# Optimization experiments

Hardware: AMD Instinct MI355X
Metric: run time of the kernel (lower is better)

Reference implementation:

```python
import jax, jax.numpy as jnp
import numpy as np

NUM_NODES = 100000
NUM_EDGES = 640000
IN_DIM = 128
OUT_DIM = 128
NUM_REL = 16


def setup_inputs() -> dict:
    key = jax.random.key(0)
    k1, k2, k3, k4, k5 = jax.random.split(key, 5)
    x = jax.random.normal(k1, (NUM_NODES, IN_DIM), dtype=jnp.float32)
    edge_index = jax.random.randint(k2, (2, NUM_EDGES), 0, NUM_NODES, dtype=jnp.int64)
    edge_types = jax.random.randint(k3, (NUM_EDGES,), 0, NUM_REL, dtype=jnp.int64)
    # xavier-uniform-ish params
    rw_bound = float(np.sqrt(6.0 / (IN_DIM * OUT_DIM + NUM_REL)))
    relation_weights = jax.random.uniform(k4, (NUM_REL, IN_DIM, OUT_DIM), dtype=jnp.float32, minval=-rw_bound, maxval=rw_bound)
    sw_bound = float(np.sqrt(6.0 / (IN_DIM + OUT_DIM)))
    self_weight = jax.random.uniform(k5, (IN_DIM, OUT_DIM), dtype=jnp.float32, minval=-sw_bound, maxval=sw_bound)
    bias = jnp.zeros((OUT_DIM,), dtype=jnp.float32)
    return {
        'x': x,
        'edge_index': edge_index,
        'edge_types': edge_types,
        'relation_weights': relation_weights,
        'self_weight': self_weight,
        'bias': bias,
    }


def reference(x, edge_index, edge_types, relation_weights, self_weight, bias):
    num_nodes = x.shape[0]
    # self loop transform: (N, out)
    self_msg = x @ self_weight
    # transform all nodes by every relation weight once: (R, N, out)
    transformed = jnp.einsum('ni,rio->rno', x, relation_weights)
    src = edge_index[0]
    dst = edge_index[1]
    # per-edge message: pick (relation, source) transformed feature -> (E, out)
    msgs = transformed[edge_types, src]
    # scatter-add into destination nodes
    neighbor_msg = jax.ops.segment_sum(msgs, dst, num_segments=num_nodes)
    # dropout=0.0 (eval) -> identity
    return jax.nn.relu(self_msg + neighbor_msg + bias)
```

## Files before the change

kernel.cpp:

```cpp
#include <hip/hip_runtime.h>

#define N_NODES 100000
#define N_EDGES 640000
#define IN_DIM  128
#define OUT_DIM 128
#define N_REL   16
#define EPB     64
#define MEPB    128
#define PAD     2048
#define NB_SCAN ((N_NODES + 255) / 256)
#define CVT_XB  (N_NODES * IN_DIM / 4 / 256)
#define CVT_WB  (17 * 16384 / 256)
#define HIST_B  ((N_EDGES + 255) / 256)

typedef unsigned short u16;
typedef unsigned int   u32;
typedef __attribute__((ext_vector_type(8))) short bf16x8;
typedef __attribute__((ext_vector_type(4))) float f32x4;

__device__ inline u16 f2bf(float f) {
    u32 u = __builtin_bit_cast(u32, f);
    return (u16)((u + 0x7fffu + ((u >> 16) & 1u)) >> 16);
}
__device__ inline float bf2f(u16 s) {
    u32 u = ((u32)s) << 16;
    return __builtin_bit_cast(float, u);
}

__global__ __launch_bounds__(256) void k_pre(const float* __restrict__ x,
                                             const float* __restrict__ rw,
                                             const float* __restrict__ sw,
                                             const int* __restrict__ etype,
                                             const int* __restrict__ dst,
                                             u16* __restrict__ xb,
                                             u16* __restrict__ wt,
                                             int* __restrict__ counts_rel,
                                             int* __restrict__ dst_count) {
    int b = blockIdx.x, t = threadIdx.x;
    if (b < CVT_XB) {
        int i = b * 256 + t;
        float4 v = ((const float4*)x)[i];
        ushort4 p; p.x = f2bf(v.x); p.y = f2bf(v.y); p.z = f2bf(v.z); p.w = f2bf(v.w);
        ((ushort4*)xb)[i] = p;
    } else if (b < CVT_XB + CVT_WB) {
        int i = (b - CVT_XB) * 256 + t;
        int r = i >> 14, rem = i & 16383, n = rem & 127;
        float v = (r < 16) ? rw[i] : sw[rem];
        int k = rem >> 7;
        wt[(size_t)r * 16384 + n * 128 + k] = f2bf(v);
    } else {
        __shared__ int bins[N_REL];
        if (t < N_REL) bins[t] = 0;
        __syncthreads();
        int e = (b - CVT_XB - CVT_WB) * 256 + t;
        if (e < N_EDGES) {
            atomicAdd(&bins[etype[e]], 1);
            atomicAdd(&dst_count[dst[e]], 1);
        }
        __syncthreads();
        if (t < N_REL && bins[t]) atomicAdd(&counts_rel[t], bins[t]);
    }
}

__global__ __launch_bounds__(256) void k_scan1(const int* __restrict__ dst_count,
                                               int* __restrict__ row_ptr,
                                               int* __restrict__ part) {
    __shared__ int buf[2][256];
    int t = threadIdx.x;
    int i = blockIdx.x * 256 + t;
    int v = (i < N_NODES) ? dst_count[i] : 0;
    buf[0][t] = v;
    __syncthreads();
    int cur = 0;
    #pragma unroll
    for (int off = 1; off < 256; off <<= 1) {
        int nxt = cur ^ 1;
        int s = buf[cur][t];
        if (t >= off) s += buf[cur][t - off];
        buf[nxt][t] = s;
        __syncthreads();
        cur = nxt;
    }
    int inc = buf[cur][t];
    if (i < N_NODES) row_ptr[i] = inc - v;
    if (t == 255) part[blockIdx.x] = inc;
}

__global__ __launch_bounds__(512) void k_mid2(int* __restrict__ part,
                                              const int* __restrict__ counts,
                                              int* __restrict__ cursor,
                                              int* __restrict__ seg,
                                              int* __restrict__ sorted) {
    int t = threadIdx.x;
    if (blockIdx.x == 0) {
        __shared__ int buf[2][512];
        int v = (t < NB_SCAN) ? part[t] : 0;
        buf[0][t] = v;
        __syncthreads();
        int cur = 0;
        #pragma unroll
        for (int off = 1; off < 512; off <<= 1) {
            int nxt = cur ^ 1;
            int s = buf[cur][t];
            if (t >= off) s += buf[cur][t - off];
            buf[nxt][t] = s;
            __syncthreads();
            cur = nxt;
        }
        int inc = buf[cur][t];
        if (t < NB_SCAN) part[t] = inc - v;
    } else {
        __shared__ int s_seg[N_REL + 1];
        if (t == 0) {
            int s = 0;
            for (int r = 0; r < N_REL; ++r) {
                cursor[r] = s; seg[r] = s; s_seg[r] = s;
                s += (counts[r] + 127) & ~127;
            }
            seg[N_REL] = s; s_seg[N_REL] = s;
        }
        __syncthreads();
        for (int r = 0; r < N_REL; ++r) {
            int b = s_seg[r] + counts[r], e2 = s_seg[r + 1];
            if (b + t < e2) sorted[b + t] = N_EDGES + r;
        }
        for (int i = s_seg[N_REL] + t; i < N_EDGES + PAD; i += 512)
            sorted[i] = N_EDGES + (N_REL - 1);
    }
}

__global__ __launch_bounds__(256) void k_scan3(int* __restrict__ row_ptr,
                                               const int* __restrict__ part,
                                               int* __restrict__ cursor_dst) {
    int t = threadIdx.x;
    int i = blockIdx.x * 256 + t;
    if (i < N_NODES) {
        int r = row_ptr[i] + part[blockIdx.x];
        row_ptr[i] = r;
        cursor_dst[i] = r;
    }
    if (i == 0) row_ptr[N_NODES] = N_EDGES;
}

__global__ __launch_bounds__(256) void k_scatter_pos(const int* __restrict__ etype,
                                                     const int* __restrict__ dst,
                                                     int* __restrict__ cursor_rel,
                                                     int* __restrict__ cursor_dst,
                                                     int* __restrict__ sorted,
                                                     int* __restrict__ pos) {
    __shared__ int bins[N_REL];
    __shared__ int base[N_REL];
    int t = threadIdx.x;
    if (t < N_REL) bins[t] = 0;
    __syncthreads();
    int e = blockIdx.x * 256 + t;
    int rel = 0;
    bool valid = (e < N_EDGES);
    if (valid) { rel = etype[e]; atomicAdd(&bins[rel], 1); }
    __syncthreads();
    if (t < N_REL) {
        base[t] = bins[t] ? atomicAdd(&cursor_rel[t], bins[t]) : 0;
        bins[t] = 0;
    }
    __syncthreads();
    if (valid) {
        int slot = base[rel] + atomicAdd(&bins[rel], 1);
        sorted[slot] = e;
        pos[slot] = atomicAdd(&cursor_dst[dst[e]], 1);
    }
}

__global__ __launch_bounds__(256, 4) void k_self_mfma(const u16* __restrict__ xb,
                                                      const u16* __restrict__ wt,
                                                      const float* __restrict__ bias,
                                                      float* __restrict__ out) {
    int t = threadIdx.x;
    int w = t >> 6, lane = t & 63;
    int n = lane & 15, q = lane >> 4;
    int n0 = blockIdx.x * 256 + w * 64;
    const u16* wr = wt + (size_t)16 * 16384;

    bf16x8 bx[4][4];
    int node[4];
    #pragma unroll
    for (int g = 0; g < 4; ++g) {
        node[g] = n0 + g * 16 + n;
        int rn = node[g] < N_NODES ? node[g] : N_NODES - 1;
        const u16* xrow = xb + (size_t)rn * 128 + q * 8;
        #pragma unroll
        for (int kk = 0; kk < 4; ++kk)
            bx[g][kk] = *(const bf16x8*)(xrow + kk * 32);
    }
    #pragma unroll
    for (int c = 0; c < 8; ++c) {
        bf16x8 aw[4];
        const u16* wrow = wr + (c * 16 + n) * 128 + q * 8;
        #pragma unroll
        for (int kk = 0; kk < 4; ++kk)
            aw[kk] = *(const bf16x8*)(wrow + kk * 32);
        float4 b4 = *(const float4*)&bias[c * 16 + q * 4];
        #pragma unroll
        for (int g = 0; g < 4; ++g) {
            f32x4 acc = {0.f, 0.f, 0.f, 0.f};
            #pragma unroll
            for (int kk = 0; kk < 4; ++kk)
                acc = __builtin_amdgcn_mfma_f32_16x16x32_bf16(aw[kk], bx[g][kk], acc, 0, 0, 0);
            if (node[g] < N_NODES) {
                float4 o;
                o.x = acc[0] + b4.x; o.y = acc[1] + b4.y;
                o.z = acc[2] + b4.z; o.w = acc[3] + b4.w;
                *(float4*)&out[(size_t)node[g] * 128 + c * 16 + q * 4] = o;
            }
        }
    }
}

__global__ __launch_bounds__(256, 4) void k_msg_mfma(const u16* __restrict__ xb,
                                                     const u16* __restrict__ wt,
                                                     const int* __restrict__ src,
                                                     const int* __restrict__ etype,
                                                     const int* __restrict__ sorted,
                                                     const int* __restrict__ pos,
                                                     u16* __restrict__ msgs) {
    __shared__ u16 s_w[128 * 136];
    __shared__ int s_src[MEPB], s_pos[MEPB];
    int t = threadIdx.x;
    int e0 = blockIdx.x * MEPB;

    int ee = sorted[e0];
    int relb = (ee < N_EDGES) ? etype[ee] : (ee - N_EDGES);
    const uint4* wsrc = (const uint4*)(wt + (size_t)relb * 16384);
    for (int i = t; i < 2048; i += 256) {
        uint4 v = wsrc[i];
        *(uint4*)&s_w[(i >> 4) * 136 + (i & 15) * 8] = v;
    }
    if (t < MEPB) {
        int eid = sorted[e0 + t];
        if (eid < N_EDGES) {
            s_src[t] = src[eid];
            s_pos[t] = pos[e0 + t];
        } else {
            s_src[t] = 0;
            s_pos[t] = N_EDGES + ((e0 + t) & (PAD - 1));
        }
    }
    __syncthreads();

    int wv = t >> 6, lane = t & 63;
    int n = lane & 15, q = lane >> 4;
    int eb = wv * 32;

    bf16x8 bx[2][4];
    int p[2];
    #pragma unroll
    for (int g = 0; g < 2; ++g) {
        int en = eb + g * 16 + n;
        const u16* xrow = xb + (size_t)s_src[en] * 128 + q * 8;
        p[g] = s_pos[en];
        #pragma unroll
        for (int kk = 0; kk < 4; ++kk)
            bx[g][kk] = *(const bf16x8*)(xrow + kk * 32);
    }

    uint4 uv[2][4];
    #pragma unroll
    for (int c = 0; c < 8; ++c) {
        bf16x8 aw[4];
        const u16* wrow = &s_w[(c * 16 + n) * 136 + q * 8];
        #pragma unroll
        for (int kk = 0; kk < 4; ++kk)
            aw[kk] = *(const bf16x8*)(wrow + kk * 32);
        #pragma unroll
        for (int g = 0; g < 2; ++g) {
            f32x4 acc = {0.f, 0.f, 0.f, 0.f};
            #pragma unroll
            for (int kk = 0; kk < 4; ++kk)
                acc = __builtin_amdgcn_mfma_f32_16x16x32_bf16(aw[kk], bx[g][kk], acc, 0, 0, 0);
            u32 lo = (u32)f2bf(acc[0]) | ((u32)f2bf(acc[1]) << 16);
            u32 hi = (u32)f2bf(acc[2]) | ((u32)f2bf(acc[3]) << 16);
            if ((c & 1) == 0) { uv[g][c >> 1].x = lo; uv[g][c >> 1].y = hi; }
            else              { uv[g][c >> 1].z = lo; uv[g][c >> 1].w = hi; }
        }
    }
    #pragma unroll
    for (int g = 0; g < 2; ++g) {
        u32* mrow = (u32*)(msgs + (size_t)p[g] * 128 + q * 32);
        #pragma unroll
        for (int j = 0; j < 4; ++j)
            *(uint4*)(mrow + j * 4) = uv[g][j];
    }
}

__global__ __launch_bounds__(256) void k_gather(const int* __restrict__ row_ptr,
                                                const u16* __restrict__ msgs,
                                                float* __restrict__ out) {
    int wid  = (blockIdx.x * 256 + threadIdx.x) >> 6;
    int lane = threadIdx.x & 63;
    if (wid >= N_NODES) return;
    int r0 = row_ptr[wid], r1 = row_ptr[wid + 1];
    int h = lane & 15, quarter = lane >> 4;
    const uint4* m = (const uint4*)msgs;
    float s[8] = {0.f,0.f,0.f,0.f,0.f,0.f,0.f,0.f};
    for (int i = r0 + quarter; i < r1; i += 4) {
        uint4 v = m[(size_t)i * 16 + h];
        s[0] += bf2f((u16)(v.x & 0xffffu)); s[1] += bf2f((u16)(v.x >> 16));
        s[2] += bf2f((u16)(v.y & 0xffffu)); s[3] += bf2f((u16)(v.y >> 16));
        s[4] += bf2f((u16)(v.z & 0xffffu)); s[5] += bf2f((u16)(v.z >> 16));
        s[6] += bf2f((u16)(v.w & 0xffffu)); s[7] += bf2f((u16)(v.w >> 16));
    }
    #pragma unroll
    for (int j = 0; j < 8; ++j) {
        s[j] += __shfl_xor(s[j], 16);
        s[j] += __shfl_xor(s[j], 32);
    }
    if (quarter == 0) {
        int c0 = (2 * h) & 7, c1 = (2 * h + 1) & 7, qq = h >> 2;
        float* ob = out + (size_t)wid * 128;
        float4* o0 = (float4*)(ob + c0 * 16 + qq * 4);
        float4* o1 = (float4*)(ob + c1 * 16 + qq * 4);
        float4 v0 = *o0, v1 = *o1;
        v0.x = fmaxf(v0.x + s[0], 0.f); v0.y = fmaxf(v0.y + s[1], 0.f);
        v0.z = fmaxf(v0.z + s[2], 0.f); v0.w = fmaxf(v0.w + s[3], 0.f);
        v1.x = fmaxf(v1.x + s[4], 0.f); v1.y = fmaxf(v1.y + s[5], 0.f);
        v1.z = fmaxf(v1.z + s[6], 0.f); v1.w = fmaxf(v1.w + s[7], 0.f);
        *o0 = v0; *o1 = v1;
    }
}

__global__ __launch_bounds__(128) void k_self_old(const float* __restrict__ x,
                                                  const float* __restrict__ sw,
                                                  const float* __restrict__ bias,
                                                  float* __restrict__ out) {
    __shared__ float s_x[8][IN_DIM];
    int t = threadIdx.x;
    int n0 = blockIdx.x * 8;
    for (int i = t; i < 8 * IN_DIM; i += 128) {
        int r = i >> 7, j = i & 127;
        s_x[r][j] = x[(size_t)(n0 + r) * IN_DIM + j];
    }
    __syncthreads();
    float acc[8] = {0.f,0.f,0.f,0.f,0.f,0.f,0.f,0.f};
    for (int k = 0; k < IN_DIM; ++k) {
        float w = sw[k * OUT_DIM + t];
        #pragma unroll
        for (int i = 0; i < 8; ++i) acc[i] += s_x[i][k] * w;
    }
    float b = bias[t];
    #pragma unroll
    for (int i = 0; i < 8; ++i)
        out[(size_t)(n0 + i) * OUT_DIM + t] = acc[i] + b;
}

__global__ __launch_bounds__(256) void k_hist_rel(const int* __restrict__ etype,
                                                  int* __restrict__ counts_rel) {
    __shared__ int bins[N_REL];
    int t = threadIdx.x;
    if (t < N_REL) bins[t] = 0;
    __syncthreads();
    int e = blockIdx.x * 256 + t;
    if (e < N_EDGES) atomicAdd(&bins[etype[e]], 1);
    __syncthreads();
    if (t < N_REL && bins[t]) atomicAdd(&counts_rel[t], bins[t]);
}

__global__ void k_scan_rel(const int* __restrict__ counts, int* __restrict__ cursor) {
    if (threadIdx.x == 0) {
        int s = 0;
        for (int r = 0; r < N_REL; ++r) { cursor[r] = s; s += counts[r]; }
    }
}

__global__ __launch_bounds__(256) void k_scatter_rel(const int* __restrict__ etype,
                                                     int* __restrict__ cursor,
                                                     int* __restrict__ sorted) {
    __shared__ int bins[N_REL];
    __shared__ int base[N_REL];
    int t = threadIdx.x;
    if (t < N_REL) bins[t] = 0;
    __syncthreads();
    int e = blockIdx.x * 256 + t;
    int rel = 0;
    bool valid = (e < N_EDGES);
    if (valid) { rel = etype[e]; atomicAdd(&bins[rel], 1); }
    __syncthreads();
    if (t < N_REL) {
        base[t] = bins[t] ? atomicAdd(&cursor[t], bins[t]) : 0;
        bins[t] = 0;
    }
    __syncthreads();
    if (valid) {
        int p = atomicAdd(&bins[rel], 1);
        sorted[base[rel] + p] = e;
    }
}

__global__ __launch_bounds__(256) void k_edge_atomic(const float* __restrict__ x,
                                              const float* __restrict__ rw,
                                              const int* __restrict__ src,
                                              const int* __restrict__ dst,
                                              const int* __restrict__ etype,
                                              const int* __restrict__ sorted,
                                              float* __restrict__ out) {
    __shared__ int s_src[EPB], s_dst[EPB], s_rel[EPB];
    __shared__ float s_x[EPB][IN_DIM];
    int t = threadIdx.x;
    int e0 = blockIdx.x * EPB;
    if (t < EPB) {
        int eid = sorted[e0 + t];
        s_src[t] = src[eid]; s_dst[t] = dst[eid]; s_rel[t] = etype[eid];
    }
    __syncthreads();
    for (int i = t; i < EPB * IN_DIM; i += 256) {
        int e = i >> 7, j = i & 127;
        s_x[e][j] = x[(size_t)s_src[e] * IN_DIM + j];
    }
    int rel0 = s_rel[0];
    bool uni = true;
    for (int i = 1; i < EPB; ++i) uni &= (s_rel[i] == rel0);
    __syncthreads();
    int cg = t & 31, eg = t >> 5;
    for (int i = 0; i < 8; ++i) {
        int e = eg * 8 + i;
        int rel = uni ? rel0 : s_rel[e];
        const float4* Wr = (const float4*)(rw + (size_t)rel * IN_DIM * OUT_DIM);
        float a0=0.f, a1=0.f, a2=0.f, a3=0.f;
        for (int k = 0; k < 128; ++k) {
            float4 w = Wr[k * 32 + cg];
            float xv = s_x[e][k];
            a0 += xv * w.x; a1 += xv * w.y; a2 += xv * w.z; a3 += xv * w.w;
        }
        float* o = out + (size_t)s_dst[e] * OUT_DIM + cg * 4;
        atomicAdd(o + 0, a0); atomicAdd(o + 1, a1);
        atomicAdd(o + 2, a2); atomicAdd(o + 3, a3);
    }
}

__global__ void k_relu(float* __restrict__ out) {
    int i = blockIdx.x * blockDim.x + threadIdx.x;
    float4* o4 = (float4*)out;
    const int n4 = N_NODES * OUT_DIM / 4;
    if (i < n4) {
        float4 v = o4[i];
        v.x = fmaxf(v.x, 0.f); v.y = fmaxf(v.y, 0.f);
        v.z = fmaxf(v.z, 0.f); v.w = fmaxf(v.w, 0.f);
        o4[i] = v;
    }
}

extern "C" void kernel_launch(void* const* d_in, const int* in_sizes, int n_in,
                              void* d_out, int out_size, void* d_ws, size_t ws_size,
                              hipStream_t stream) {
    const float* x     = (const float*)d_in[0];
    const int*   eidx  = (const int*)d_in[1];
    const int*   etype = (const int*)d_in[2];
    const float* rw    = (const float*)d_in[3];
    const float* sw    = (const float*)d_in[4];
    const float* bias  = (const float*)d_in[5];
    float* out = (float*)d_out;
    const int* src = eidx;
    const int* dst = eidx + N_EDGES;

    int* counts_rel = (int*)d_ws;
    int* cursor_rel = counts_rel + 16;
    int* seg        = cursor_rel + 16;
    int* part       = seg + 32;
    int* dst_count  = part + 512;
    int* row_ptr    = dst_count + N_NODES;
    int* cursor_dst = row_ptr + N_NODES + 1;
    int* sorted     = cursor_dst + N_NODES;
    int* pos        = sorted + N_EDGES + PAD;
    size_t off = (((char*)(pos + N_EDGES + PAD) - (char*)d_ws) + 255) & ~(size_t)255;
    u16* xb   = (u16*)((char*)d_ws + off);
    u16* wtb  = xb + (size_t)N_NODES * 128;
    u16* msgs = wtb + 17 * 16384;
    size_t need = (size_t)((char*)(msgs + (size_t)(N_EDGES + PAD) * 128) - (char*)d_ws);

    const int EB = HIST_B;
    const int MB = (N_EDGES + PAD) / MEPB;

    if (ws_size >= need) {
        hipMemsetAsync(d_ws, 0, (size_t)(576 + N_NODES) * sizeof(int), stream);
        k_pre<<<CVT_XB + CVT_WB + EB, 256, 0, stream>>>(x, rw, sw, etype, dst,
                                                        xb, wtb, counts_rel, dst_count);
        k_scan1<<<NB_SCAN, 256, 0, stream>>>(dst_count, row_ptr, part);
        k_mid2<<<2, 512, 0, stream>>>(part, counts_rel, cursor_rel, seg, sorted);
        k_scan3<<<NB_SCAN, 256, 0, stream>>>(row_ptr, part, cursor_dst);
        k_scatter_pos<<<EB, 256, 0, stream>>>(etype, dst, cursor_rel, cursor_dst, sorted, pos);

        k_self_mfma<<<(N_NODES + 255) / 256, 256, 0, stream>>>(xb, wtb, bias, out);
        k_msg_mfma<<<MB, 256, 0, stream>>>(xb, wtb, src, etype, sorted, pos, msgs);
        k_gather<<<(N_NODES * 64 + 255) / 256, 256, 0, stream>>>(row_ptr, msgs, out);
    } else {
        hipMemsetAsync(counts_rel, 0, 16 * sizeof(int), stream);
        k_hist_rel<<<EB, 256, 0, stream>>>(etype, counts_rel);
        k_scan_rel<<<1, 64, 0, stream>>>(counts_rel, cursor_rel);
        k_scatter_rel<<<EB, 256, 0, stream>>>(etype, cursor_rel, sorted);
        k_self_old<<<N_NODES / 8, 128, 0, stream>>>(x, sw, bias, out);
        k_edge_atomic<<<N_EDGES / EPB, 256, 0, stream>>>(x, rw, src, dst, etype, sorted, out);
        k_relu<<<(N_NODES * OUT_DIM / 4 + 255) / 256, 256, 0, stream>>>(out);
    }
}
```

Baseline: 369.2 us.

## Fold self-loop transform into message MFMA as 17th relation and pre-swizzle weights

```diff
diff --git a/kernel.cpp b/kernel.cpp
--- a/kernel.cpp
+++ b/kernel.cpp
@@ -7,11 +7,15 @@
 #define N_REL   16
 #define EPB     64
 #define MEPB    128
-#define PAD     2048
+#define SELF_PAD 100096
+#define MAX_SLOTS (SELF_PAD + N_EDGES + 2048)
+#define SENT    (N_EDGES + N_NODES)
+#define MSG_ROWS (N_EDGES + N_NODES + 128)
 #define NB_SCAN ((N_NODES + 255) / 256)
 #define CVT_XB  (N_NODES * IN_DIM / 4 / 256)
 #define CVT_WB  (17 * 16384 / 256)
 #define HIST_B  ((N_EDGES + 255) / 256)
+#define SELF_B  (SELF_PAD / 256)
 
 typedef unsigned short u16;
 typedef unsigned int   u32;
@@ -35,7 +39,8 @@
                                              u16* __restrict__ xb,
                                              u16* __restrict__ wt,
                                              int* __restrict__ counts_rel,
-                                             int* __restrict__ dst_count) {
+                                             int* __restrict__ dst_count,
+                                             int* __restrict__ sorted) {
     int b = blockIdx.x, t = threadIdx.x;
     if (b < CVT_XB) {
         int i = b * 256 + t;
@@ -44,11 +49,12 @@
         ((ushort4*)xb)[i] = p;
     } else if (b < CVT_XB + CVT_WB) {
         int i = (b - CVT_XB) * 256 + t;
-        int r = i >> 14, rem = i & 16383, n = rem & 127;
+        int r = i >> 14, rem = i & 16383;
+        int k = rem >> 7, np = rem & 127;
         float v = (r < 16) ? rw[i] : sw[rem];
-        int k = rem >> 7;
-        wt[(size_t)r * 16384 + n * 128 + k] = f2bf(v);
-    } else {
+        int c = np >> 4, nn = np & 15, kk = k >> 5, q = (k >> 3) & 3, j = k & 7;
+        wt[(size_t)r * 16384 + (c * 4 + kk) * 512 + (q * 16 + nn) * 8 + j] = f2bf(v);
+    } else if (b < CVT_XB + CVT_WB + HIST_B) {
         __shared__ int bins[N_REL];
         if (t < N_REL) bins[t] = 0;
         __syncthreads();
@@ -59,6 +65,9 @@
         }
         __syncthreads();
         if (t < N_REL && bins[t]) atomicAdd(&counts_rel[t], bins[t]);
+    } else {
+        int i = (b - CVT_XB - CVT_WB - HIST_B) * 256 + t;
+        sorted[i] = (i < N_NODES) ? (N_EDGES + i) : SENT;
     }
 }
 
@@ -68,7 +77,7 @@
     __shared__ int buf[2][256];
     int t = threadIdx.x;
     int i = blockIdx.x * 256 + t;
-    int v = (i < N_NODES) ? dst_count[i] : 0;
+    int v = (i < N_NODES) ? (dst_count[i] + 1) : 0;
     buf[0][t] = v;
     __syncthreads();
     int cur = 0;
@@ -112,7 +121,7 @@
     } else {
         __shared__ int s_seg[N_REL + 1];
         if (t == 0) {
-            int s = 0;
+            int s = SELF_PAD;
             for (int r = 0; r < N_REL; ++r) {
                 cursor[r] = s; seg[r] = s; s_seg[r] = s;
                 s += (counts[r] + 127) & ~127;
@@ -122,10 +131,10 @@
         __syncthreads();
         for (int r = 0; r < N_REL; ++r) {
             int b = s_seg[r] + counts[r], e2 = s_seg[r + 1];
-            if (b + t < e2) sorted[b + t] = N_EDGES + r;
-        }
-        for (int i = s_seg[N_REL] + t; i < N_EDGES + PAD; i += 512)
-            sorted[i] = N_EDGES + (N_REL - 1);
+            if (b + t < e2) sorted[b + t] = SENT;
+        }
+        for (int i = s_seg[N_REL] + t; i < MAX_SLOTS; i += 512)
+            sorted[i] = SENT;
     }
 }
 
@@ -137,17 +146,14 @@
     if (i < N_NODES) {
         int r = row_ptr[i] + part[blockIdx.x];
         row_ptr[i] = r;
-        cursor_dst[i] = r;
-    }
-    if (i == 0) row_ptr[N_NODES] = N_EDGES;
-}
-
-__global__ __launch_bounds__(256) void k_scatter_pos(const int* __restrict__ etype,
-                                                     const int* __restrict__ dst,
-                                                     int* __restrict__ cursor_rel,
-                                                     int* __restrict__ cursor_dst,
-                                                     int* __restrict__ sorted,
-                                                     int* __restrict__ pos) {
+        cursor_dst[i] = r + 1;
+    }
+    if (i == 0) row_ptr[N_NODES] = N_EDGES + N_NODES;
+}
+
+__global__ __launch_bounds__(256) void k_scatter_rel(const int* __restrict__ etype,
+                                                     int* __restrict__ cursor,
+                                                     int* __restrict__ sorted) {
     __shared__ int bins[N_REL];
     __shared__ int base[N_REL];
     int t = threadIdx.x;
@@ -159,59 +165,13 @@
     if (valid) { rel = etype[e]; atomicAdd(&bins[rel], 1); }
     __syncthreads();
     if (t < N_REL) {
-        base[t] = bins[t] ? atomicAdd(&cursor_rel[t], bins[t]) : 0;
+        base[t] = bins[t] ? atomicAdd(&cursor[t], bins[t]) : 0;
         bins[t] = 0;
     }
     __syncthreads();
     if (valid) {
-        int slot = base[rel] + atomicAdd(&bins[rel], 1);
-        sorted[slot] = e;
-        pos[slot] = atomicAdd(&cursor_dst[dst[e]], 1);
-    }
-}
-
-__global__ __launch_bounds__(256, 4) void k_self_mfma(const u16* __restrict__ xb,
-                                                      const u16* __restrict__ wt,
-                                                      const float* __restrict__ bias,
-                                                      float* __restrict__ out) {
-    int t = threadIdx.x;
-    int w = t >> 6, lane = t & 63;
-    int n = lane & 15, q = lane >> 4;
-    int n0 = blockIdx.x * 256 + w * 64;
-    const u16* wr = wt + (size_t)16 * 16384;
-
-    bf16x8 bx[4][4];
-    int node[4];
-    #pragma unroll
-    for (int g = 0; g < 4; ++g) {
-        node[g] = n0 + g * 16 + n;
-        int rn = node[g] < N_NODES ? node[g] : N_NODES - 1;
-        const u16* xrow = xb + (size_t)rn * 128 + q * 8;
-        #pragma unroll
-        for (int kk = 0; kk < 4; ++kk)
-            bx[g][kk] = *(const bf16x8*)(xrow + kk * 32);
-    }
-    #pragma unroll
-    for (int c = 0; c < 8; ++c) {
-        bf16x8 aw[4];
-        const u16* wrow = wr + (c * 16 + n) * 128 + q * 8;
-        #pragma unroll
-        for (int kk = 0; kk < 4; ++kk)
-            aw[kk] = *(const bf16x8*)(wrow + kk * 32);
-        float4 b4 = *(const float4*)&bias[c * 16 + q * 4];
-        #pragma unroll
-        for (int g = 0; g < 4; ++g) {
-            f32x4 acc = {0.f, 0.f, 0.f, 0.f};
-            #pragma unroll
-            for (int kk = 0; kk < 4; ++kk)
-                acc = __builtin_amdgcn_mfma_f32_16x16x32_bf16(aw[kk], bx[g][kk], acc, 0, 0, 0);
-            if (node[g] < N_NODES) {
-                float4 o;
-                o.x = acc[0] + b4.x; o.y = acc[1] + b4.y;
-                o.z = acc[2] + b4.z; o.w = acc[3] + b4.w;
-                *(float4*)&out[(size_t)node[g] * 128 + c * 16 + q * 4] = o;
-            }
-        }
+        int p = atomicAdd(&bins[rel], 1);
+        sorted[base[rel] + p] = e;
     }
 }
 
@@ -219,30 +179,35 @@
                                                      const u16* __restrict__ wt,
                                                      const int* __restrict__ src,
                                                      const int* __restrict__ etype,
+                                                     const int* __restrict__ dst,
                                                      const int* __restrict__ sorted,
-                                                     const int* __restrict__ pos,
+                                                     const int* __restrict__ row_ptr,
+                                                     int* __restrict__ cursor_dst,
                                                      u16* __restrict__ msgs) {
-    __shared__ u16 s_w[128 * 136];
+    __shared__ u16 s_w[128 * 128];
     __shared__ int s_src[MEPB], s_pos[MEPB];
     int t = threadIdx.x;
     int e0 = blockIdx.x * MEPB;
 
-    int ee = sorted[e0];
-    int relb = (ee < N_EDGES) ? etype[ee] : (ee - N_EDGES);
+    int ee0 = sorted[e0];
+    int relb = (ee0 < N_EDGES) ? etype[ee0] : N_REL;
     const uint4* wsrc = (const uint4*)(wt + (size_t)relb * 16384);
-    for (int i = t; i < 2048; i += 256) {
-        uint4 v = wsrc[i];
-        *(uint4*)&s_w[(i >> 4) * 136 + (i & 15) * 8] = v;
-    }
+    for (int i = t; i < 2048; i += 256)
+        *(uint4*)&s_w[i * 8] = wsrc[i];
     if (t < MEPB) {
         int eid = sorted[e0 + t];
+        int sv, pv;
         if (eid < N_EDGES) {
-            s_src[t] = src[eid];
-            s_pos[t] = pos[e0 + t];
+            sv = src[eid];
+            pv = atomicAdd(&cursor_dst[dst[eid]], 1);
+        } else if (eid < SENT) {
+            sv = eid - N_EDGES;
+            pv = row_ptr[sv];
         } else {
-            s_src[t] = 0;
-            s_pos[t] = N_EDGES + ((e0 + t) & (PAD - 1));
-        }
+            sv = 0;
+            pv = SENT + ((e0 + t) & 127);
+        }
+        s_src[t] = sv; s_pos[t] = pv;
     }
     __syncthreads();
 
@@ -266,10 +231,9 @@
     #pragma unroll
     for (int c = 0; c < 8; ++c) {
         bf16x8 aw[4];
-        const u16* wrow = &s_w[(c * 16 + n) * 136 + q * 8];
         #pragma unroll
         for (int kk = 0; kk < 4; ++kk)
-            aw[kk] = *(const bf16x8*)(wrow + kk * 32);
+            aw[kk] = *(const bf16x8*)&s_w[(c * 4 + kk) * 512 + lane * 8];
         #pragma unroll
         for (int g = 0; g < 2; ++g) {
             f32x4 acc = {0.f, 0.f, 0.f, 0.f};
@@ -293,6 +257,7 @@
 
 __global__ __launch_bounds__(256) void k_gather(const int* __restrict__ row_ptr,
                                                 const u16* __restrict__ msgs,
+                                                const float* __restrict__ bias,
                                                 float* __restrict__ out) {
     int wid  = (blockIdx.x * 256 + threadIdx.x) >> 6;
     int lane = threadIdx.x & 63;
@@ -315,15 +280,16 @@
     }
     if (quarter == 0) {
         int c0 = (2 * h) & 7, c1 = (2 * h + 1) & 7, qq = h >> 2;
+        float4 b0 = *(const float4*)&bias[c0 * 16 + qq * 4];
+        float4 b1 = *(const float4*)&bias[c1 * 16 + qq * 4];
         float* ob = out + (size_t)wid * 128;
-        float4* o0 = (float4*)(ob + c0 * 16 + qq * 4);
-        float4* o1 = (float4*)(ob + c1 * 16 + qq * 4);
-        float4 v0 = *o0, v1 = *o1;
-        v0.x = fmaxf(v0.x + s[0], 0.f); v0.y = fmaxf(v0.y + s[1], 0.f);
-        v0.z = fmaxf(v0.z + s[2], 0.f); v0.w = fmaxf(v0.w + s[3], 0.f);
-        v1.x = fmaxf(v1.x + s[4], 0.f); v1.y = fmaxf(v1.y + s[5], 0.f);
-        v1.z = fmaxf(v1.z + s[6], 0.f); v1.w = fmaxf(v1.w + s[7], 0.f);
-        *o0 = v0; *o1 = v1;
+        float4 v0, v1;
+        v0.x = fmaxf(s[0] + b0.x, 0.f); v0.y = fmaxf(s[1] + b0.y, 0.f);
+        v0.z = fmaxf(s[2] + b0.z, 0.f); v0.w = fmaxf(s[3] + b0.w, 0.f);
+        v1.x = fmaxf(s[4] + b1.x, 0.f); v1.y = fmaxf(s[5] + b1.y, 0.f);
+        v1.z = fmaxf(s[6] + b1.z, 0.f); v1.w = fmaxf(s[7] + b1.w, 0.f);
+        *(float4*)(ob + c0 * 16 + qq * 4) = v0;
+        *(float4*)(ob + c1 * 16 + qq * 4) = v1;
     }
 }
 
@@ -367,30 +333,6 @@
     if (threadIdx.x == 0) {
         int s = 0;
         for (int r = 0; r < N_REL; ++r) { cursor[r] = s; s += counts[r]; }
-    }
-}
-
-__global__ __launch_bounds__(256) void k_scatter_rel(const int* __restrict__ etype,
-                                                     int* __restrict__ cursor,
-                                                     int* __restrict__ sorted) {
-    __shared__ int bins[N_REL];
-    __shared__ int base[N_REL];
-    int t = threadIdx.x;
-    if (t < N_REL) bins[t] = 0;
-    __syncthreads();
-    int e = blockIdx.x * 256 + t;
-    int rel = 0;
-    bool valid = (e < N_EDGES);
-    if (valid) { rel = etype[e]; atomicAdd(&bins[rel], 1); }
-    __syncthreads();
-    if (t < N_REL) {
-        base[t] = bins[t] ? atomicAdd(&cursor[t], bins[t]) : 0;
-        bins[t] = 0;
-    }
-    __syncthreads();
-    if (valid) {
-        int p = atomicAdd(&bins[rel], 1);
-        sorted[base[rel] + p] = e;
     }
 }
 
@@ -468,33 +410,31 @@
     int* row_ptr    = dst_count + N_NODES;
     int* cursor_dst = row_ptr + N_NODES + 1;
     int* sorted     = cursor_dst + N_NODES;
-    int* pos        = sorted + N_EDGES + PAD;
-    size_t off = (((char*)(pos + N_EDGES + PAD) - (char*)d_ws) + 255) & ~(size_t)255;
+    size_t off = (((char*)(sorted + MAX_SLOTS) - (char*)d_ws) + 255) & ~(size_t)255;
     u16* xb   = (u16*)((char*)d_ws + off);
     u16* wtb  = xb + (size_t)N_NODES * 128;
     u16* msgs = wtb + 17 * 16384;
-    size_t need = (size_t)((char*)(msgs + (size_t)(N_EDGES + PAD) * 128) - (char*)d_ws);
-
-    const int EB = HIST_B;
-    const int MB = (N_EDGES + PAD) / MEPB;
+    size_t need = (size_t)((char*)(msgs + (size_t)MSG_ROWS * 128) - (char*)d_ws);
+
+    const int MB = MAX_SLOTS / MEPB;
 
     if (ws_size >= need) {
         hipMemsetAsync(d_ws, 0, (size_t)(576 + N_NODES) * sizeof(int), stream);
-        k_pre<<<CVT_XB + CVT_WB + EB, 256, 0, stream>>>(x, rw, sw, etype, dst,
-                                                        xb, wtb, counts_rel, dst_count);
+        k_pre<<<CVT_XB + CVT_WB + HIST_B + SELF_B, 256, 0, stream>>>(
+            x, rw, sw, etype, dst, xb, wtb, counts_rel, dst_count, sorted);
         k_scan1<<<NB_SCAN, 256, 0, stream>>>(dst_count, row_ptr, part);
         k_mid2<<<2, 512, 0, stream>>>(part, counts_rel, cursor_rel, seg, sorted);
         k_scan3<<<NB_SCAN, 256, 0, stream>>>(row_ptr, part, cursor_dst);
-        k_scatter_pos<<<EB, 256, 0, stream>>>(etype, dst, cursor_rel, cursor_dst, sorted, pos);
-
-        k_self_mfma<<<(N_NODES + 255) / 256, 256, 0, stream>>>(xb, wtb, bias, out);
-        k_msg_mfma<<<MB, 256, 0, stream>>>(xb, wtb, src, etype, sorted, pos, msgs);
-        k_gather<<<(N_NODES * 64 + 255) / 256, 256, 0, stream>>>(row_ptr, msgs, out);
+        k_scatter_rel<<<HIST_B, 256, 0, stream>>>(etype, cursor_rel, sorted);
+
+        k_msg_mfma<<<MB, 256, 0, stream>>>(xb, wtb, src, etype, dst, sorted,
+                                           row_ptr, cursor_dst, msgs);
+        k_gather<<<(N_NODES * 64 + 255) / 256, 256, 0, stream>>>(row_ptr, msgs, bias, out);
     } else {
         hipMemsetAsync(counts_rel, 0, 16 * sizeof(int), stream);
-        k_hist_rel<<<EB, 256, 0, stream>>>(etype, counts_rel);
+        k_hist_rel<<<HIST_B, 256, 0, stream>>>(etype, counts_rel);
         k_scan_rel<<<1, 64, 0, stream>>>(counts_rel, cursor_rel);
-        k_scatter_rel<<<EB, 256, 0, stream>>>(etype, cursor_rel, sorted);
+        k_scatter_rel<<<HIST_B, 256, 0, stream>>>(etype, cursor_rel, sorted);
         k_self_old<<<N_NODES / 8, 128, 0, stream>>>(x, sw, bias, out);
         k_edge_atomic<<<N_EDGES / EPB, 256, 0, stream>>>(x, rw, src, dst, etype, sorted, out);
         k_relu<<<(N_NODES * OUT_DIM / 4 + 255) / 256, 256, 0, stream>>>(out);
```

Result: faster. 322.5 us (-12.6%).
